# Kernel tuning notes

Measured on AMD Instinct MI355X. Metric: run time of the kernel, lower is better.

The kernel has to match this reference:

```python
import jax, jax.numpy as jnp
import numpy as np

LN_EPS = 1e-5


def _gather(x, idx):
    # x: [B, N, C], idx: [B, N, K] -> [B, N, K, C]
    return jax.vmap(lambda xb, ib: xb[ib])(x, idx)


def setup_inputs() -> dict:
    key = jax.random.key(0)
    ks = jax.random.split(key, 8)
    B, N, K, C_in, C_out, GEO = 2, 16384, 32, 128, 128, 10
    return {
        "points": jax.random.normal(ks[0], (B, N, 3), dtype=jnp.float32),
        "features": jax.random.normal(ks[1], (B, N, C_in), dtype=jnp.float32),
        "grouped_idx": jax.random.randint(ks[2], (B, N, K), 0, N, dtype=jnp.int32),
        "w_pos": jax.random.normal(ks[3], (GEO, C_in), dtype=jnp.float32) * (GEO ** -0.5),
        "b_pos": jnp.zeros((C_in,), jnp.float32),
        "w_gcm": jax.random.normal(ks[4], (C_in, C_in), dtype=jnp.float32) * (C_in ** -0.5),
        "b_gcm": jnp.zeros((C_in,), jnp.float32),
        "w_out": jax.random.normal(ks[5], (C_in, C_out), dtype=jnp.float32) * (C_in ** -0.5),
        "b_out": jnp.zeros((C_out,), jnp.float32),
        "ln_g": jnp.ones((C_out,), jnp.float32),
        "ln_b": jnp.zeros((C_out,), jnp.float32),
    }


def reference(points, features, grouped_idx, w_pos, b_pos, w_gcm, b_gcm,
              w_out, b_out, ln_g, ln_b):
    # gather neighbor coords and features: [B, N, K, *]
    grouped_pts = _gather(points, grouped_idx)
    xyz = points[..., 0:3]                      # [B, N, 3]
    grouped_xyz = grouped_pts[..., 0:3]         # [B, N, K, 3]
    center = xyz[:, :, None, :]                 # [B, N, 1, 3]
    diff = grouped_xyz - center                 # xi - xj
    dist = jnp.linalg.norm(diff, axis=-1, keepdims=True)  # ||xi - xj||
    K = grouped_xyz.shape[2]
    geo = jnp.concatenate(
        [jnp.broadcast_to(center, grouped_xyz.shape), grouped_xyz, diff, dist],
        axis=-1)                                # [B, N, K, 10]
    expanded_f = geo @ w_pos + b_pos            # pos_proj -> [B, N, K, C_in]
    grouped_f = _gather(features, grouped_idx)  # [B, N, K, C_in]
    h = jax.nn.relu((grouped_f + expanded_f) @ w_gcm + b_gcm)  # gcm_layer
    pooled = jnp.max(h, axis=2)                 # maxpooling over neighbors
    res = pooled + features                     # residual
    o = res @ w_out + b_out                     # out Linear
    mu = jnp.mean(o, axis=-1, keepdims=True)
    var = jnp.mean((o - mu) ** 2, axis=-1, keepdims=True)
    o = (o - mu) * jax.lax.rsqrt(var + LN_EPS) * ln_g + ln_b  # LayerNorm
    return jax.nn.relu(o)
```

## Files before the change

kernel.cpp:

```cpp
#include <hip/hip_runtime.h>
#include <hip/hip_bf16.h>
#include <math.h>

typedef __attribute__((ext_vector_type(8))) short short8;
typedef __attribute__((ext_vector_type(4))) short short4v;
typedef __attribute__((ext_vector_type(4))) float float4v;
typedef __attribute__((ext_vector_type(2))) unsigned int uint2v;
typedef unsigned short ushort_t;

constexpr int NPTS = 32768;
constexpr int NN   = 16384;
constexpr int KK   = 32;
constexpr int CC   = 128;
constexpr int GRP  = 16;
constexpr int SR   = 136;
constexpr int SG2  = 24;
#define LN_EPS 1e-5f
#define MFMA   __builtin_amdgcn_mfma_f32_16x16x32_bf16
#define GLL(src, dst, sz) __builtin_amdgcn_global_load_lds( \
    (const __attribute__((address_space(1))) void*)(src),   \
    (__attribute__((address_space(3))) void*)(dst), sz, 0, 0)

constexpr size_t WS_FW  = 0;
constexpr size_t WS_WO  = (size_t)NPTS * CC * 2;
constexpr size_t WS_BE  = WS_WO + 32768;
constexpr size_t WS_WPF = WS_BE + 512;
constexpr size_t WS_PG  = WS_WPF + 32768;
constexpr size_t WS_NEED = WS_PG + 5120;
constexpr size_t FB_WP = 0, FB_WO = 40960, FB_BE = 73728, FB_PG = 74240;

__device__ __forceinline__ short f2bs(float x) {
    return (short)__builtin_bit_cast(unsigned short, __float2bfloat16(x));
}
__device__ __forceinline__ float bs2f(ushort_t u) {
    return __uint_as_float(((unsigned)u) << 16);
}

__global__ __launch_bounds__(256) void prep1(
    const float* __restrict__ w_gcm, const float* __restrict__ w_out,
    const float* __restrict__ w_pos, const float* __restrict__ b_pos,
    const float* __restrict__ b_gcm,
    short* __restrict__ wsWpF, short* __restrict__ wsWo,
    float* __restrict__ wsBeff, float* __restrict__ wsPG)
{
    const int t = threadIdx.x, blk = blockIdx.x;
    if (blk == 0) {
        #pragma unroll 4
        for (int e = t; e < 16 * 128 * 8; e += 256) {
            const int j = e & 7, n = (e >> 3) & 127, g = e >> 10;
            wsWpF[e] = f2bs(w_gcm[(g * 8 + j) * 128 + n]);
        }
    } else if (blk == 1) {
        #pragma unroll 4
        for (int e = t; e < 128 * 128; e += 256) {
            const int j = e & 7, n = (e >> 3) & 127, g = e >> 10;
            wsWo[e] = f2bs(w_out[(g * 8 + j) * 128 + n]);
        }
    } else if (blk < 12) {
        if (t < 128) {
            const int g = blk - 2, c = t;
            float s = 0.f;
            #pragma unroll
            for (int r = 0; r < 128; ++r) s += w_pos[g * 128 + r] * w_gcm[r * 128 + c];
            wsPG[g * 128 + c] = s;
        }
    } else {
        if (t < 128) {
            const int c = t;
            float sb = b_gcm[c];
            #pragma unroll
            for (int r = 0; r < 128; ++r) sb += b_pos[r] * w_gcm[r * 128 + c];
            wsBeff[c] = sb;
        }
    }
}

__global__ __launch_bounds__(256) void prep_fw(
    const float* __restrict__ features, const short* __restrict__ wsWpF,
    ushort_t* __restrict__ wsFW)
{
    const int t = threadIdx.x, blk = blockIdx.x;
    __shared__ short sF[16 * SR];
    const int g0 = blk * GRP;
    {
        const int row = t >> 4, c8 = (t & 15) * 8;
        const float* fp = features + (size_t)(g0 + row) * CC + c8;
        const float4 a = *(const float4*)fp;
        const float4 b = *(const float4*)(fp + 4);
        short8 v;
        v[0]=f2bs(a.x); v[1]=f2bs(a.y); v[2]=f2bs(a.z); v[3]=f2bs(a.w);
        v[4]=f2bs(b.x); v[5]=f2bs(b.y); v[6]=f2bs(b.z); v[7]=f2bs(b.w);
        *(short8*)&sF[row * SR + c8] = v;
    }
    const int wv = t >> 6, lane = t & 63, quad = (lane >> 4) & 3, m = lane & 15;
    const int col0 = wv * 32 + m;
    short8 bf[4][2];
    #pragma unroll
    for (int ks = 0; ks < 4; ++ks) {
        bf[ks][0] = *((const short8*)wsWpF + ((ks * 4 + quad) * 128 + col0));
        bf[ks][1] = *((const short8*)wsWpF + ((ks * 4 + quad) * 128 + col0 + 16));
    }
    __syncthreads();
    float4v acc[2] = {};
    #pragma unroll
    for (int ks = 0; ks < 4; ++ks) {
        const short8 a = *(const short8*)(sF + m * SR + ks * 32 + quad * 8);
        acc[0] = MFMA(a, bf[ks][0], acc[0], 0, 0, 0);
        acc[1] = MFMA(a, bf[ks][1], acc[1], 0, 0, 0);
    }
    #pragma unroll
    for (int r = 0; r < 4; ++r) {
        const int R = quad * 4 + r;
        wsFW[(size_t)(g0 + R) * CC + col0]      = (ushort_t)f2bs(acc[0][r]);
        wsFW[(size_t)(g0 + R) * CC + col0 + 16] = (ushort_t)f2bs(acc[1][r]);
    }
}

__global__ __launch_bounds__(256, 4) void bridge_fw(
    const float* __restrict__ points, const float* __restrict__ features,
    const int*   __restrict__ gidx,
    const short* __restrict__ wsWo, const float* __restrict__ wsBeff,
    const float* __restrict__ wsPG, const ushort_t* __restrict__ wsFW,
    const float* __restrict__ b_out, const float* __restrict__ ln_g,
    const float* __restrict__ ln_b, float* __restrict__ out)
{
    __shared__ short sA[4][3][1024];
    __shared__ short sGeo[GRP * KK * 4];
    __shared__ short sRes[GRP * SR];
    __shared__ float sCtr[GRP * 3];
    __shared__ float sPS[4][GRP], sPQ[4][GRP];

    const int t = threadIdx.x, wv = t >> 6, lane = t & 63;
    const int q = (lane >> 4) & 3, m = lane & 15;
    const int g0 = blockIdx.x * GRP;
    const int nbase = (g0 >= NN) ? NN : 0;
    const int colA = wv * 32 + m;
    const int rbL = lane >> 3, jL = (lane & 7) >> 1, hL = lane & 1;

    #pragma unroll
    for (int rep = 0; rep < 2; ++rep) {
        const int e = t + rep * 256;
        const int p = e >> 5;
        const int gA = gidx[(size_t)g0 * KK + e];
        const float* pn = points + (size_t)(nbase + gA) * 3;
        const float* pcp = points + (size_t)(g0 + p) * 3;
        const float ax = pn[0], ay = pn[1], az = pn[2];
        const float dx = ax - pcp[0], dy = ay - pcp[1], dz = az - pcp[2];
        const float ds = sqrtf(dx * dx + dy * dy + dz * dz);
        short4v v; v[0]=f2bs(ax); v[1]=f2bs(ay); v[2]=f2bs(az); v[3]=f2bs(ds);
        *(short4v*)&sGeo[e * 4] = v;
    }
    if (t < GRP * 3) sCtr[t] = points[(size_t)g0 * 3 + t];

    int kwReg[GRP];
    {
        const int offL = rbL * 4 + jL;
        #pragma unroll
        for (int p = 0; p < GRP; ++p)
            kwReg[p] = nbase + gidx[(size_t)g0 * KK + p * KK + offL];
    }

    float rr[4][2];
    #pragma unroll
    for (int j = 0; j < 4; ++j) {
        const size_t pt = (size_t)(g0 + q * 4 + j) * CC;
        rr[j][0] = features[pt + colA];
        rr[j][1] = features[pt + colA + 16];
    }

    const float beffv[2] = { wsBeff[colA], wsBeff[colA + 16] };
    float wc[6];
    short8 w4f[2];
    #pragma unroll
    for (int n = 0; n < 2; ++n) {
        const int c = colA + n * 16;
        const float p0 = wsPG[0*128+c], p1 = wsPG[1*128+c], p2 = wsPG[2*128+c];
        const float p3 = wsPG[3*128+c], p4 = wsPG[4*128+c], p5 = wsPG[5*128+c];
        const float p6 = wsPG[6*128+c], p7 = wsPG[7*128+c], p8 = wsPG[8*128+c];
        const float p9 = wsPG[9*128+c];
        wc[n*3+0] = p0 - p6; wc[n*3+1] = p1 - p7; wc[n*3+2] = p2 - p8;
        short8 w = (short8)0;
        w[0] = f2bs(p3 + p6); w[1] = f2bs(p4 + p7); w[2] = f2bs(p5 + p8); w[3] = f2bs(p9);
        w4f[n] = (q == 0) ? w : (short8)0;
    }
    const unsigned trBase = (unsigned)(size_t)(__attribute__((address_space(3))) short*)&sA[wv][0][0]
                          + (unsigned)(lane * 8);

    __syncthreads();

    auto issue_fw = [&](int p, int buf) {
        const ushort_t* s0 = wsFW + (size_t)kwReg[p] * CC + wv * 32 + hL * 8;
        GLL(s0,      &sA[wv][buf][0],   16);
        GLL(s0 + 16, &sA[wv][buf][512], 16);
    };

    issue_fw(0, 0);
    issue_fw(1, 1);

    float cbv[GRP][2];
    #pragma unroll
    for (int p = 0; p < GRP; ++p) {
        const float cx = sCtr[p * 3], cy = sCtr[p * 3 + 1], cz = sCtr[p * 3 + 2];
        cbv[p][0] = cx * wc[0] + cy * wc[1] + cz * wc[2];
        cbv[p][1] = cx * wc[3] + cy * wc[4] + cz * wc[5];
    }

    #pragma unroll
    for (int p = 0; p < GRP; ++p) {
        const int buf = p % 3;
        if (p + 2 < GRP) issue_fw(p + 2, (p + 2) % 3);
        if (p + 2 < GRP)      asm volatile("s_waitcnt vmcnt(4)" ::: "memory");
        else if (p + 1 < GRP) asm volatile("s_waitcnt vmcnt(2)" ::: "memory");
        else                  asm volatile("s_waitcnt vmcnt(0)" ::: "memory");
        __builtin_amdgcn_sched_barrier(0x6);

        uint2v t00, t10, t01, t11;
        const unsigned trA = trBase + (unsigned)(buf * 2048);
        asm volatile("ds_read_b64_tr_b16 %0, %1 offset:0"    : "=&v"(t00) : "v"(trA));
        asm volatile("ds_read_b64_tr_b16 %0, %1 offset:512"  : "=&v"(t10) : "v"(trA));
        asm volatile("ds_read_b64_tr_b16 %0, %1 offset:1024" : "=&v"(t01) : "v"(trA));
        asm volatile("ds_read_b64_tr_b16 %0, %1 offset:1536" : "=&v"(t11) : "v"(trA));

        short8 ga0 = (short8)0, ga1 = (short8)0;
        if (q == 0) {
            const short4v gA0 = *(const short4v*)&sGeo[(p * KK + m) * 4];
            const short4v gA1 = *(const short4v*)&sGeo[(p * KK + 16 + m) * 4];
            ga0[0]=gA0[0]; ga0[1]=gA0[1]; ga0[2]=gA0[2]; ga0[3]=gA0[3];
            ga1[0]=gA1[0]; ga1[1]=gA1[1]; ga1[2]=gA1[2]; ga1[3]=gA1[3];
        }

        asm volatile("s_waitcnt lgkmcnt(0)" ::: "memory");
        __builtin_amdgcn_sched_barrier(0);

        __builtin_amdgcn_s_setprio(1);
        float4v c00, c10, c01, c11;
        c00[0]=__uint_as_float(t00[0] << 16); c00[1]=__uint_as_float(t00[0] & 0xffff0000u);
        c00[2]=__uint_as_float(t00[1] << 16); c00[3]=__uint_as_float(t00[1] & 0xffff0000u);
        c10[0]=__uint_as_float(t10[0] << 16); c10[1]=__uint_as_float(t10[0] & 0xffff0000u);
        c10[2]=__uint_as_float(t10[1] << 16); c10[3]=__uint_as_float(t10[1] & 0xffff0000u);
        c01[0]=__uint_as_float(t01[0] << 16); c01[1]=__uint_as_float(t01[0] & 0xffff0000u);
        c01[2]=__uint_as_float(t01[1] << 16); c01[3]=__uint_as_float(t01[1] & 0xffff0000u);
        c11[0]=__uint_as_float(t11[0] << 16); c11[1]=__uint_as_float(t11[0] & 0xffff0000u);
        c11[2]=__uint_as_float(t11[1] << 16); c11[3]=__uint_as_float(t11[1] & 0xffff0000u);

        c00 = MFMA(ga0, w4f[0], c00, 0, 0, 0);
        c01 = MFMA(ga0, w4f[1], c01, 0, 0, 0);
        c10 = MFMA(ga1, w4f[0], c10, 0, 0, 0);
        c11 = MFMA(ga1, w4f[1], c11, 0, 0, 0);
        __builtin_amdgcn_s_setprio(0);

        float v0 = fmaxf(fmaxf(fmaxf(c00[0], c00[1]), fmaxf(c00[2], c00[3])),
                         fmaxf(fmaxf(c10[0], c10[1]), fmaxf(c10[2], c10[3])));
        float v1 = fmaxf(fmaxf(fmaxf(c01[0], c01[1]), fmaxf(c01[2], c01[3])),
                         fmaxf(fmaxf(c11[0], c11[1]), fmaxf(c11[2], c11[3])));
        v0 = fmaxf(v0, __shfl_xor(v0, 16)); v0 = fmaxf(v0, __shfl_xor(v0, 32));
        v1 = fmaxf(v1, __shfl_xor(v1, 16)); v1 = fmaxf(v1, __shfl_xor(v1, 32));
        v0 = fmaxf(v0 + beffv[0] + cbv[p][0], 0.f);
        v1 = fmaxf(v1 + beffv[1] + cbv[p][1], 0.f);

        const float fc0 = __shfl(rr[p & 3][0], ((p >> 2) << 4) + m);
        const float fc1 = __shfl(rr[p & 3][1], ((p >> 2) << 4) + m);
        if (q == 0) {
            sRes[p * SR + colA]      = f2bs(v0 + fc0);
            sRes[p * SR + colA + 16] = f2bs(v1 + fc1);
        }
    }

    __syncthreads();

    short8 bWo[4][2];
    #pragma unroll
    for (int ks = 0; ks < 4; ++ks)
        #pragma unroll
        for (int ntl = 0; ntl < 2; ++ntl)
            bWo[ks][ntl] = *((const short8*)wsWo + ((ks * 4 + q) * 128 + colA + ntl * 16));

    const short* rm = sRes + m * SR;
    float4v acc2[2] = {};
    #pragma unroll
    for (int ks = 0; ks < 4; ++ks) {
        const short8 a = *(const short8*)(rm + ks * 32 + q * 8);
        acc2[0] = MFMA(a, bWo[ks][0], acc2[0], 0, 0, 0);
        acc2[1] = MFMA(a, bWo[ks][1], acc2[1], 0, 0, 0);
    }

    const float boutv[2] = { b_out[colA], b_out[colA + 16] };
    const float lngv[2]  = { ln_g[colA], ln_g[colA + 16] };
    const float lnbv[2]  = { ln_b[colA], ln_b[colA + 16] };

    #pragma unroll
    for (int r = 0; r < 4; ++r) {
        const float o0 = acc2[0][r] + boutv[0];
        const float o1 = acc2[1][r] + boutv[1];
        float ss = o0 + o1, qq = o0 * o0 + o1 * o1;
        #pragma unroll
        for (int d = 1; d < 16; d <<= 1) { ss += __shfl_xor(ss, d); qq += __shfl_xor(qq, d); }
        if (m == 0) { sPS[wv][q * 4 + r] = ss; sPQ[wv][q * 4 + r] = qq; }
    }
    __syncthreads();

    #pragma unroll
    for (int r = 0; r < 4; ++r) {
        const int R = q * 4 + r;
        const float S = sPS[0][R] + sPS[1][R] + sPS[2][R] + sPS[3][R];
        const float Q = sPQ[0][R] + sPQ[1][R] + sPQ[2][R] + sPQ[3][R];
        const float mu  = S * (1.f / 128.f);
        const float var = fmaxf(Q * (1.f / 128.f) - mu * mu, 0.f);
        const float rstd = rsqrtf(var + LN_EPS);
        const float o0 = acc2[0][r] + boutv[0];
        const float o1 = acc2[1][r] + boutv[1];
        const size_t base = (size_t)(g0 + R) * CC;
        out[base + colA]      = fmaxf((o0 - mu) * rstd * lngv[0] + lnbv[0], 0.f);
        out[base + colA + 16] = fmaxf((o1 - mu) * rstd * lngv[1] + lnbv[1], 0.f);
    }
}

__global__ __launch_bounds__(128) void prep_fold_fb(
    const float* __restrict__ w_pos, const float* __restrict__ b_pos,
    const float* __restrict__ w_gcm, const float* __restrict__ b_gcm,
    float* __restrict__ wsPG, float* __restrict__ wsBeff)
{
    const int c = threadIdx.x, g = blockIdx.x;
    if (g < 10) {
        float s = 0.f;
        for (int r = 0; r < 128; ++r) s += w_pos[g * 128 + r] * w_gcm[r * 128 + c];
        wsPG[g * 128 + c] = s;
    } else {
        float s = b_gcm[c];
        for (int r = 0; r < 128; ++r) s += b_pos[r] * w_gcm[r * 128 + c];
        wsBeff[c] = s;
    }
}

__global__ __launch_bounds__(256) void prep_pack_fb(
    const float* __restrict__ w_gcm, const float* __restrict__ w_out,
    const float* __restrict__ wsPG, short* __restrict__ wsWp, short* __restrict__ wsWo)
{
    const int t = threadIdx.x, blk = blockIdx.x;
    if (blk == 0) {
        #pragma unroll 4
        for (int e = t; e < 16 * 128 * 8; e += 256) {
            const int j = e & 7, n = (e >> 3) & 127, g = e >> 10;
            wsWp[e] = f2bs(w_gcm[(g * 8 + j) * 128 + n]);
        }
    } else if (blk == 1) {
        #pragma unroll 4
        for (int e2 = t; e2 < 4 * 128 * 8; e2 += 256) {
            const int e = 16 * 128 * 8 + e2;
            const int j = e & 7, n = (e >> 3) & 127, g = e >> 10;
            const int k = g * 8 + j;
            wsWp[e] = (k < 138) ? f2bs(wsPG[(k - 128) * 128 + n]) : (short)0;
        }
    } else {
        #pragma unroll 4
        for (int e = t; e < 128 * 128; e += 256) {
            const int j = e & 7, n = (e >> 3) & 127, g = e >> 10;
            wsWo[e] = f2bs(w_out[(g * 8 + j) * 128 + n]);
        }
    }
}

__global__ __launch_bounds__(256, 3) void bridge_fb(
    const float* __restrict__ points, const float* __restrict__ features,
    const int*   __restrict__ gidx,
    const short* __restrict__ wsWp, const short* __restrict__ wsWo,
    const float* __restrict__ wsBeff,
    const float* __restrict__ b_out, const float* __restrict__ ln_g,
    const float* __restrict__ ln_b, float* __restrict__ out)
{
    __shared__ short sA[4][KK * CC];
    __shared__ short sG[3][KK * SG2];
    __shared__ short sRes[GRP * SR];
    __shared__ short sResF[GRP * CC];
    __shared__ int   sIdx[GRP * KK];
    __shared__ float sCtr[GRP * 3];
    __shared__ float sPS[4][GRP], sPQ[4][GRP];

    const int t = threadIdx.x, wv = t >> 6, lane = t & 63;
    const int quad = (lane >> 4) & 3, m = lane & 15;
    const int g0 = blockIdx.x * GRP;
    const int nbase = (g0 >= NN) ? NN : 0;
    const int col0 = wv * 32 + m;

    sIdx[t]       = gidx[(size_t)g0 * KK + t];
    sIdx[t + 256] = gidx[(size_t)g0 * KK + t + 256];
    if (t < GRP * 3) sCtr[t] = points[(size_t)g0 * 3 + t];
    {
        const float* fs = features + (size_t)g0 * CC + t * 8;
        short8 v;
        #pragma unroll
        for (int i = 0; i < 8; ++i) v[i] = f2bs(fs[i]);
        *(short8*)&sResF[t * 8] = v;
    }

    short8 bWp[5][2];
    #pragma unroll
    for (int ks = 0; ks < 5; ++ks)
        #pragma unroll
        for (int ntl = 0; ntl < 2; ++ntl)
            bWp[ks][ntl] = *((const short8*)wsWp + ((ks * 4 + quad) * 128 + col0 + ntl * 16));
    const float beffv[2] = { wsBeff[col0], wsBeff[col0 + 16] };

    __syncthreads();

    const int r0 = wv * 4 + (lane >> 4);
    const int pc = lane & 15;
    const int gc = pc ^ r0;

    float geoS[3][3];

    auto geo_load = [&](int qq) {
        if (lane < 8) {
            const int j = wv * 8 + lane;
            const int kng = nbase + sIdx[qq * KK + j];
            const float* pp = points + (size_t)kng * 3;
            const int s = qq % 3;
            geoS[s][0] = pp[0]; geoS[s][1] = pp[1]; geoS[s][2] = pp[2];
        }
    };
    auto stage = [&](int qq) {
        const int buf = qq & 3;
        const int kn0 = nbase + sIdx[qq * KK + r0];
        const int kn1 = nbase + sIdx[qq * KK + r0 + 16];
        const float4* f0 = (const float4*)(features + (size_t)kn0 * CC + gc * 8);
        const float4* f1 = (const float4*)(features + (size_t)kn1 * CC + gc * 8);
        const float4 a = f0[0], b = f0[1], c = f1[0], d = f1[1];
        short8 v;
        v[0]=f2bs(a.x); v[1]=f2bs(a.y); v[2]=f2bs(a.z); v[3]=f2bs(a.w);
        v[4]=f2bs(b.x); v[5]=f2bs(b.y); v[6]=f2bs(b.z); v[7]=f2bs(b.w);
        *(short8*)&sA[buf][r0 * CC + pc * 8] = v;
        v[0]=f2bs(c.x); v[1]=f2bs(c.y); v[2]=f2bs(c.z); v[3]=f2bs(c.w);
        v[4]=f2bs(d.x); v[5]=f2bs(d.y); v[6]=f2bs(d.z); v[7]=f2bs(d.w);
        *(short8*)&sA[buf][(r0 + 16) * CC + pc * 8] = v;
    };
    auto geo_store = [&](int qq) {
        if (lane < 8) {
            const int j = wv * 8 + lane, s = qq % 3, b = qq % 3;
            const float cx = sCtr[qq * 3], cy = sCtr[qq * 3 + 1], cz = sCtr[qq * 3 + 2];
            const float gx = geoS[s][0], gy = geoS[s][1], gz = geoS[s][2];
            const float dx = gx - cx, dy = gy - cy, dz = gz - cz;
            const float dist = sqrtf(dx * dx + dy * dy + dz * dz);
            short8 v0, v1 = (short8)0;
            v0[0]=f2bs(cx); v0[1]=f2bs(cy); v0[2]=f2bs(cz);
            v0[3]=f2bs(gx); v0[4]=f2bs(gy); v0[5]=f2bs(gz);
            v0[6]=f2bs(dx); v0[7]=f2bs(dy);
            v1[0]=f2bs(dz); v1[1]=f2bs(dist);
            *(short8*)&sG[b][j * SG2 + 0] = v0;
            *(short8*)&sG[b][j * SG2 + 8] = v1;
        }
    };

    int offA[4];
    #pragma unroll
    for (int ks = 0; ks < 4; ++ks) offA[ks] = m * CC + (((ks * 4 + quad) ^ m) * 8);
    const int offG = m * SG2 + quad * 8;

    geo_load(0); stage(0);
    geo_load(1); stage(1);
    geo_load(2); stage(2);
    geo_store(0); geo_store(1);
    __syncthreads();

    #pragma unroll
    for (int p = 0; p < GRP; ++p) {
        if (p > 0) {
            asm volatile("s_waitcnt lgkmcnt(0)" ::: "memory");
            __builtin_amdgcn_s_barrier();
        }
        __builtin_amdgcn_sched_barrier(0);
        if (p + 3 < GRP) { geo_load(p + 3); stage(p + 3); }

        const short* ab = sA[p & 3];
        const short* ag = sG[p % 3];
        float4v acc[2][2] = {};
        #pragma unroll
        for (int ks = 0; ks < 4; ++ks) {
            const short8 a0 = *(const short8*)(ab + offA[ks]);
            const short8 a1 = *(const short8*)(ab + offA[ks] + 16 * CC);
            acc[0][0] = MFMA(a0, bWp[ks][0], acc[0][0], 0, 0, 0);
            acc[0][1] = MFMA(a0, bWp[ks][1], acc[0][1], 0, 0, 0);
            acc[1][0] = MFMA(a1, bWp[ks][0], acc[1][0], 0, 0, 0);
            acc[1][1] = MFMA(a1, bWp[ks][1], acc[1][1], 0, 0, 0);
        }
        short8 ga0 = (short8)0, ga1 = (short8)0;
        if (quad < 2) {
            ga0 = *(const short8*)(ag + offG);
            ga1 = *(const short8*)(ag + offG + 16 * SG2);
        }
        acc[0][0] = MFMA(ga0, bWp[4][0], acc[0][0], 0, 0, 0);
        acc[0][1] = MFMA(ga0, bWp[4][1], acc[0][1], 0, 0, 0);
        acc[1][0] = MFMA(ga1, bWp[4][0], acc[1][0], 0, 0, 0);
        acc[1][1] = MFMA(ga1, bWp[4][1], acc[1][1], 0, 0, 0);

        #pragma unroll
        for (int ntl = 0; ntl < 2; ++ntl) {
            float v = acc[0][ntl][0];
            #pragma unroll
            for (int rr2 = 1; rr2 < 4; ++rr2) v = fmaxf(v, acc[0][ntl][rr2]);
            #pragma unroll
            for (int rr2 = 0; rr2 < 4; ++rr2) v = fmaxf(v, acc[1][ntl][rr2]);
            v = fmaxf(v, __shfl_xor(v, 16));
            v = fmaxf(v, __shfl_xor(v, 32));
            v = fmaxf(v + beffv[ntl], 0.f);
            if (quad == 0) {
                const float fc = bs2f((ushort_t)sResF[p * CC + col0 + ntl * 16]);
                sRes[p * SR + col0 + ntl * 16] = f2bs(v + fc);
            }
        }
        if (p + 2 < GRP) geo_store(p + 2);
    }

    __syncthreads();

    short8 bWo[4][2];
    #pragma unroll
    for (int ks = 0; ks < 4; ++ks)
        #pragma unroll
        for (int ntl = 0; ntl < 2; ++ntl)
            bWo[ks][ntl] = *((const short8*)wsWo + ((ks * 4 + quad) * 128 + col0 + ntl * 16));

    const short* rm = sRes + m * SR;
    float4v acc2[2] = {};
    #pragma unroll
    for (int ks = 0; ks < 4; ++ks) {
        const short8 a = *(const short8*)(rm + ks * 32 + quad * 8);
        acc2[0] = MFMA(a, bWo[ks][0], acc2[0], 0, 0, 0);
        acc2[1] = MFMA(a, bWo[ks][1], acc2[1], 0, 0, 0);
    }
    const float boutv[2] = { b_out[col0], b_out[col0 + 16] };
    const float lngv[2]  = { ln_g[col0], ln_g[col0 + 16] };
    const float lnbv[2]  = { ln_b[col0], ln_b[col0 + 16] };
    #pragma unroll
    for (int r = 0; r < 4; ++r) {
        const float o0 = acc2[0][r] + boutv[0];
        const float o1 = acc2[1][r] + boutv[1];
        float ss = o0 + o1, qq2 = o0 * o0 + o1 * o1;
        #pragma unroll
        for (int d = 1; d < 16; d <<= 1) { ss += __shfl_xor(ss, d); qq2 += __shfl_xor(qq2, d); }
        if (m == 0) { sPS[wv][quad * 4 + r] = ss; sPQ[wv][quad * 4 + r] = qq2; }
    }
    __syncthreads();
    #pragma unroll
    for (int r = 0; r < 4; ++r) {
        const int R = quad * 4 + r;
        const float S = sPS[0][R] + sPS[1][R] + sPS[2][R] + sPS[3][R];
        const float Q = sPQ[0][R] + sPQ[1][R] + sPQ[2][R] + sPQ[3][R];
        const float mu  = S * (1.f / 128.f);
        const float var = fmaxf(Q * (1.f / 128.f) - mu * mu, 0.f);
        const float rstd = rsqrtf(var + LN_EPS);
        const float o0 = acc2[0][r] + boutv[0];
        const float o1 = acc2[1][r] + boutv[1];
        const size_t base = (size_t)(g0 + R) * CC;
        out[base + col0]      = fmaxf((o0 - mu) * rstd * lngv[0] + lnbv[0], 0.f);
        out[base + col0 + 16] = fmaxf((o1 - mu) * rstd * lngv[1] + lnbv[1], 0.f);
    }
}

extern "C" void kernel_launch(void* const* d_in, const int* in_sizes, int n_in,
                              void* d_out, int out_size, void* d_ws, size_t ws_size,
                              hipStream_t stream) {
    const float* points   = (const float*)d_in[0];
    const float* features = (const float*)d_in[1];
    const int*   gidx     = (const int*)  d_in[2];
    const float* w_pos    = (const float*)d_in[3];
    const float* b_pos    = (const float*)d_in[4];
    const float* w_gcm    = (const float*)d_in[5];
    const float* b_gcm    = (const float*)d_in[6];
    const float* w_out    = (const float*)d_in[7];
    const float* b_out    = (const float*)d_in[8];
    const float* ln_g     = (const float*)d_in[9];
    const float* ln_b     = (const float*)d_in[10];
    float* out = (float*)d_out;
    char* ws = (char*)d_ws;

    if (ws_size >= WS_NEED) {
        ushort_t* wsFW   = (ushort_t*)(ws + WS_FW);
        short*    wsWo   = (short*)(ws + WS_WO);
        float*    wsBeff = (float*)(ws + WS_BE);
        short*    wsWpF  = (short*)(ws + WS_WPF);
        float*    wsPG   = (float*)(ws + WS_PG);
        hipLaunchKernelGGL(prep1, dim3(13), dim3(256), 0, stream,
                           w_gcm, w_out, w_pos, b_pos, b_gcm,
                           wsWpF, wsWo, wsBeff, wsPG);
        hipLaunchKernelGGL(prep_fw, dim3(NPTS / GRP), dim3(256), 0, stream,
                           features, wsWpF, wsFW);
        hipLaunchKernelGGL(bridge_fw, dim3(NPTS / GRP), dim3(256), 0, stream,
                           points, features, gidx, wsWo, wsBeff, wsPG, wsFW,
                           b_out, ln_g, ln_b, out);
    } else {
        short* wsWp   = (short*)(ws + FB_WP);
        short* wsWo   = (short*)(ws + FB_WO);
        float* wsBeff = (float*)(ws + FB_BE);
        float* wsPG   = (float*)(ws + FB_PG);
        hipLaunchKernelGGL(prep_fold_fb, dim3(11), dim3(128), 0, stream,
                           w_pos, b_pos, w_gcm, b_gcm, wsPG, wsBeff);
        hipLaunchKernelGGL(prep_pack_fb, dim3(3), dim3(256), 0, stream,
                           w_gcm, w_out, wsPG, wsWp, wsWo);
        hipLaunchKernelGGL(bridge_fb, dim3(NPTS / GRP), dim3(256), 0, stream,
                           points, features, gidx, wsWp, wsWo, wsBeff,
                           b_out, ln_g, ln_b, out);
    }
}
```

Before: 140.6 us.

## Keep neighbor geometry in registers via shuffles and raise occupancy bound

Drops the shared-memory sGeo staging buffer. Each wave now computes the packed bf16 geometry (x,y,z,dist) for its neighbors into registers and distributes it with __shfl in the per-point loop. The launch bound goes from 4 to 5 blocks per CU, relying on the smaller LDS footprint. The cost is extra registers, shuffle instructions inside the hot loop, and each wave redundantly computing the geometry gather that was previously split across the block.

```diff
diff --git a/kernel.cpp b/kernel.cpp
--- a/kernel.cpp
+++ b/kernel.cpp
@@ -116,7 +116,7 @@
     }
 }
 
-__global__ __launch_bounds__(256, 4) void bridge_fw(
+__global__ __launch_bounds__(256, 5) void bridge_fw(
     const float* __restrict__ points, const float* __restrict__ features,
     const int*   __restrict__ gidx,
     const short* __restrict__ wsWo, const float* __restrict__ wsBeff,
@@ -125,7 +125,6 @@
     const float* __restrict__ ln_b, float* __restrict__ out)
 {
     __shared__ short sA[4][3][1024];
-    __shared__ short sGeo[GRP * KK * 4];
     __shared__ short sRes[GRP * SR];
     __shared__ float sCtr[GRP * 3];
     __shared__ float sPS[4][GRP], sPQ[4][GRP];
@@ -137,18 +136,25 @@
     const int colA = wv * 32 + m;
     const int rbL = lane >> 3, jL = (lane & 7) >> 1, hL = lane & 1;
 
-    #pragma unroll
-    for (int rep = 0; rep < 2; ++rep) {
-        const int e = t + rep * 256;
-        const int p = e >> 5;
-        const int gA = gidx[(size_t)g0 * KK + e];
-        const float* pn = points + (size_t)(nbase + gA) * 3;
-        const float* pcp = points + (size_t)(g0 + p) * 3;
-        const float ax = pn[0], ay = pn[1], az = pn[2];
-        const float dx = ax - pcp[0], dy = ay - pcp[1], dz = az - pcp[2];
-        const float ds = sqrtf(dx * dx + dy * dy + dz * dz);
-        short4v v; v[0]=f2bs(ax); v[1]=f2bs(ay); v[2]=f2bs(az); v[3]=f2bs(ds);
-        *(short4v*)&sGeo[e * 4] = v;
+    int gLo[8], gHi[8];
+    {
+        const int jG = lane >> 1;
+        #pragma unroll
+        for (int r2 = 0; r2 < 8; ++r2) {
+            const int pG = (lane & 1) * 8 + r2;
+            const int gA = gidx[(size_t)g0 * KK + pG * KK + jG];
+            const float* pn  = points + (size_t)(nbase + gA) * 3;
+            const float* pcp = points + (size_t)(g0 + pG) * 3;
+            const float ax = pn[0], ay = pn[1], az = pn[2];
+            const float dx = ax - pcp[0], dy = ay - pcp[1], dz = az - pcp[2];
+            const float ds = sqrtf(dx * dx + dy * dy + dz * dz);
+            const unsigned ua = (unsigned short)(ushort_t)f2bs(ax);
+            const unsigned ub = (unsigned short)(ushort_t)f2bs(ay);
+            const unsigned uc = (unsigned short)(ushort_t)f2bs(az);
+            const unsigned ud = (unsigned short)(ushort_t)f2bs(ds);
+            gLo[r2] = (int)(ua | (ub << 16));
+            gHi[r2] = (int)(uc | (ud << 16));
+        }
     }
     if (t < GRP * 3) sCtr[t] = points[(size_t)g0 * 3 + t];
 
@@ -222,11 +228,18 @@
         asm volatile("ds_read_b64_tr_b16 %0, %1 offset:1536" : "=&v"(t11) : "v"(trA));
 
         short8 ga0 = (short8)0, ga1 = (short8)0;
-        if (q == 0) {
-            const short4v gA0 = *(const short4v*)&sGeo[(p * KK + m) * 4];
-            const short4v gA1 = *(const short4v*)&sGeo[(p * KK + 16 + m) * 4];
-            ga0[0]=gA0[0]; ga0[1]=gA0[1]; ga0[2]=gA0[2]; ga0[3]=gA0[3];
-            ga1[0]=gA1[0]; ga1[1]=gA1[1]; ga1[2]=gA1[2]; ga1[3]=gA1[3];
+        {
+            const int srcA = 2 * m + (p >> 3);
+            const int lo0 = __shfl(gLo[p & 7], srcA);
+            const int hi0 = __shfl(gHi[p & 7], srcA);
+            const int lo1 = __shfl(gLo[p & 7], srcA + 32);
+            const int hi1 = __shfl(gHi[p & 7], srcA + 32);
+            if (q == 0) {
+                ga0[0]=(short)lo0; ga0[1]=(short)(lo0>>16);
+                ga0[2]=(short)hi0; ga0[3]=(short)(hi0>>16);
+                ga1[0]=(short)lo1; ga1[1]=(short)(lo1>>16);
+                ga1[2]=(short)hi1; ga1[3]=(short)(hi1>>16);
+            }
         }
 
         asm volatile("s_waitcnt lgkmcnt(0)" ::: "memory");
```

Measured after the change: 200.5 us. +42.6%, slower.
